# Optimization experiments

Hardware: AMD Instinct MI355X
Metric: run time of the kernel (lower is better)

Reference implementation:

```python
import jax, jax.numpy as jnp
import numpy as np

EPS = 1e-15


def setup_inputs() -> dict:
    key = jax.random.key(0)
    k1, k2 = jax.random.split(key)
    B, N, M, D = 32, 512, 64, 128  # D=128 hard-coded in original (np.zeros(128))
    videos_repr = jax.random.normal(k1, (B, N, D), dtype=jnp.float32)
    sentences_repr = jax.random.normal(k2, (B, M, D), dtype=jnp.float32)
    return {"videos_repr": videos_repr, "sentences_repr": sentences_repr}


def reference(videos_repr, sentences_repr):
    """Vectorized all-pairs (training=True) path of MomentVideo.call.

    videos_repr: [B, N, D], sentences_repr: [B, M, D].
    Returns (sum_scores_videos [B,B], sum_scores_sentences [B,B]).
    """
    V, S = videos_repr, sentences_repr
    nv = jnp.linalg.norm(V, axis=-1)  # [B, N]
    ns = jnp.linalg.norm(S, axis=-1)  # [B, M]

    # Co-attention cosine-similarity matrix for every (video i, sentence j) pair.
    # C[i,j,n,m] = <V[i,n], S[j,m]> / (||V[i,n]|| * ||S[j,m]|| + eps)
    C = jnp.einsum('ind,jmd->ijnm', V, S) / (
        nv[:, None, :, None] * ns[None, :, None, :] + EPS)

    Ps = jax.nn.softmax(C, axis=3)  # softmax over sentence words (axis=1 in per-pair matrix)
    Pv = jax.nn.softmax(C, axis=2)  # softmax over video segments (axis=0 in per-pair matrix)

    # sentence_attention[i,j,n] = sum_m Ps[i,j,n,m] * S[j,m]
    A = jnp.einsum('ijnm,jmd->ijnd', Ps, S)   # [B, B, N, D]
    # video_attention[i,j,m] = sum_n Pv[i,j,n,m] * V[i,n]
    Bt = jnp.einsum('ijnm,ind->ijmd', Pv, V)  # [B, B, M, D]

    na = jnp.linalg.norm(A, axis=-1)   # [B, B, N]
    nb = jnp.linalg.norm(Bt, axis=-1)  # [B, B, M]

    # cosine(V[i,n], A[i,j,n]) and cosine(S[j,m], Bt[i,j,m])
    sv = jnp.einsum('ind,ijnd->ijn', V, A) / (nv[:, None, :] * na + EPS)
    ss = jnp.einsum('jmd,ijmd->ijm', S, Bt) / (ns[None, :, :] * nb + EPS)

    sum_scores_videos = sv.mean(axis=-1)          # [B, B], [i, j]
    sum_scores_sentences = ss.mean(axis=-1).T     # transposed as in original
    return sum_scores_videos, sum_scores_sentences
```

## Files before the change

### kernel.cpp

```cpp
#include <hip/hip_runtime.h>
#include <hip/hip_bf16.h>
#include <math.h>

#define BB 32
#define NN 512
#define MM 64
#define DD 128
#define TILE 64
#define NTILES 8

typedef __attribute__((ext_vector_type(8))) short s8v;
typedef __attribute__((ext_vector_type(4))) float f4v;
typedef __attribute__((ext_vector_type(4))) unsigned short u4v;
typedef __attribute__((ext_vector_type(8))) unsigned short u8v;

#define MFMA(a, b, c) __builtin_amdgcn_mfma_f32_16x16x32_bf16((a), (b), (c), 0, 0, 0)

__device__ inline unsigned short f2b(float f) {
  union { __hip_bfloat16 b; unsigned short u; } cv;
  cv.b = __float2bfloat16(f);
  return cv.u;
}

__device__ inline int idxV(int r, int k)  { return r * 128 + (k ^ ((r & 7) << 3)); }
__device__ inline int idx64(int r, int k) { return r * 64  + (k ^ ((r & 7) << 3)); }

struct __align__(16) PSM {
  unsigned short A[64 * 128];
  unsigned short B[128 * 64];
};

extern "C" __global__ void __launch_bounds__(512, 2)
mv_prep(const float* __restrict__ Vg, const float* __restrict__ Sg,
        unsigned short* __restrict__ VAg, unsigned short* __restrict__ VTg,
        unsigned short* __restrict__ Sbg, unsigned short* __restrict__ Gbg,
        float* __restrict__ nvg, float* __restrict__ rnvg,
        float* __restrict__ nsg, float* __restrict__ rnsg)
{
  extern __shared__ char smraw[];
  PSM& sm = *reinterpret_cast<PSM*>(smraw);
  const int t = threadIdx.x;
  const int r = t >> 3, c = t & 7;
  const int bid = blockIdx.x;

  if (bid < 256) {
    const int i = bid >> 3, tt = bid & 7;
    const float* Vr = Vg + ((size_t)i * NN + tt * TILE + r) * DD + c * 16;
    float4 f0 = reinterpret_cast<const float4*>(Vr)[0];
    float4 f1 = reinterpret_cast<const float4*>(Vr)[1];
    float4 f2 = reinterpret_cast<const float4*>(Vr)[2];
    float4 f3 = reinterpret_cast<const float4*>(Vr)[3];
    unsigned short vb16[16] = {
      f2b(f0.x), f2b(f0.y), f2b(f0.z), f2b(f0.w),
      f2b(f1.x), f2b(f1.y), f2b(f1.z), f2b(f1.w),
      f2b(f2.x), f2b(f2.y), f2b(f2.z), f2b(f2.w),
      f2b(f3.x), f2b(f3.y), f2b(f3.z), f2b(f3.w) };
    u8v lo = { vb16[0], vb16[1], vb16[2], vb16[3], vb16[4], vb16[5], vb16[6], vb16[7] };
    u8v hi = { vb16[8], vb16[9], vb16[10], vb16[11], vb16[12], vb16[13], vb16[14], vb16[15] };
    *reinterpret_cast<u8v*>(&sm.A[idxV(r, c * 16)])     = lo;
    *reinterpret_cast<u8v*>(&sm.A[idxV(r, c * 16 + 8)]) = hi;
    #pragma unroll
    for (int q = 0; q < 8; ++q) {
      const int adr = ((c * 16 + q) << 6) + (r ^ (((q ^ c) & 7) << 3));
      sm.B[adr]       = vb16[q];
      sm.B[adr + 512] = vb16[q + 8];
    }
    float s = f0.x*f0.x + f0.y*f0.y + f0.z*f0.z + f0.w*f0.w
            + f1.x*f1.x + f1.y*f1.y + f1.z*f1.z + f1.w*f1.w
            + f2.x*f2.x + f2.y*f2.y + f2.z*f2.z + f2.w*f2.w
            + f3.x*f3.x + f3.y*f3.y + f3.z*f3.z + f3.w*f3.w;
    s += __shfl_xor(s, 1, 64);
    s += __shfl_xor(s, 2, 64);
    s += __shfl_xor(s, 4, 64);
    if (c == 0) {
      const float rs = rsqrtf(s);
      nvg [i * NN + tt * TILE + r] = s * rs;
      rnvg[i * NN + tt * TILE + r] = rs;
    }
    __syncthreads();
    unsigned short* dA = VAg + (size_t)bid * 8192;
    unsigned short* dB = VTg + (size_t)bid * 8192;
    *reinterpret_cast<u8v*>(&dA[t * 8])        = *reinterpret_cast<u8v*>(&sm.A[t * 8]);
    *reinterpret_cast<u8v*>(&dA[4096 + t * 8]) = *reinterpret_cast<u8v*>(&sm.A[4096 + t * 8]);
    *reinterpret_cast<u8v*>(&dB[t * 8])        = *reinterpret_cast<u8v*>(&sm.B[t * 8]);
    *reinterpret_cast<u8v*>(&dB[4096 + t * 8]) = *reinterpret_cast<u8v*>(&sm.B[4096 + t * 8]);
  } else {
    const int j = bid - 256;
    const float* Sp = Sg + ((size_t)j * MM + r) * DD + c * 16;
    float4 f0 = reinterpret_cast<const float4*>(Sp)[0];
    float4 f1 = reinterpret_cast<const float4*>(Sp)[1];
    float4 f2 = reinterpret_cast<const float4*>(Sp)[2];
    float4 f3 = reinterpret_cast<const float4*>(Sp)[3];
    u8v lo = { f2b(f0.x), f2b(f0.y), f2b(f0.z), f2b(f0.w),
               f2b(f1.x), f2b(f1.y), f2b(f1.z), f2b(f1.w) };
    u8v hi = { f2b(f2.x), f2b(f2.y), f2b(f2.z), f2b(f2.w),
               f2b(f3.x), f2b(f3.y), f2b(f3.z), f2b(f3.w) };
    *reinterpret_cast<u8v*>(&sm.A[idxV(r, c * 16)])     = lo;
    *reinterpret_cast<u8v*>(&sm.A[idxV(r, c * 16 + 8)]) = hi;
    float s = f0.x*f0.x + f0.y*f0.y + f0.z*f0.z + f0.w*f0.w
            + f1.x*f1.x + f1.y*f1.y + f1.z*f1.z + f1.w*f1.w
            + f2.x*f2.x + f2.y*f2.y + f2.z*f2.z + f2.w*f2.w
            + f3.x*f3.x + f3.y*f3.y + f3.z*f3.z + f3.w*f3.w;
    s += __shfl_xor(s, 1, 64);
    s += __shfl_xor(s, 2, 64);
    s += __shfl_xor(s, 4, 64);
    if (c == 0) {
      const float rs = rsqrtf(s);
      nsg [j * MM + r] = s * rs;
      rnsg[j * MM + r] = rs;
    }
    __syncthreads();
    {
      const int lane = t & 63, w = t >> 6, l15 = lane & 15, g = lane >> 4;
      const int nb = w >> 1, hf = w & 1, cB0 = hf * 32 + l15, cB1 = cB0 + 16;
      f4v g0 = {0.f,0.f,0.f,0.f}, g1 = {0.f,0.f,0.f,0.f};
      #pragma unroll
      for (int ks = 0; ks < 4; ++ks) {
        s8v a  = *reinterpret_cast<const s8v*>(&sm.A[idxV(nb * 16 + l15, ks * 32 + g * 8)]);
        s8v b0 = *reinterpret_cast<const s8v*>(&sm.A[idxV(cB0,          ks * 32 + g * 8)]);
        s8v b1 = *reinterpret_cast<const s8v*>(&sm.A[idxV(cB1,          ks * 32 + g * 8)]);
        g0 = MFMA(a, b0, g0);
        g1 = MFMA(a, b1, g1);
      }
      #pragma unroll
      for (int q = 0; q < 4; ++q) {
        const int row = nb * 16 + g * 4 + q;
        sm.B[idx64(row, cB0)] = f2b(g0[q]);
        sm.B[idx64(row, cB1)] = f2b(g1[q]);
      }
    }
    __syncthreads();
    unsigned short* dS = Sbg + (size_t)j * 8192;
    *reinterpret_cast<u8v*>(&dS[r * 128 + c * 16])     = *reinterpret_cast<u8v*>(&sm.A[idxV(r, c * 16)]);
    *reinterpret_cast<u8v*>(&dS[r * 128 + c * 16 + 8]) = *reinterpret_cast<u8v*>(&sm.A[idxV(r, c * 16 + 8)]);
    unsigned short* dG = Gbg + (size_t)j * 4096;
    *reinterpret_cast<u8v*>(&dG[r * 64 + c * 8]) = *reinterpret_cast<u8v*>(&sm.B[idx64(r, c * 8)]);
  }
}

struct __align__(16) SMem2 {
  unsigned short VA[8192];
  unsigned short VT[8192];
  unsigned short Eb[4096];
  unsigned short ET[4096];
  float RSV[32 * 68];
  float RQP[32 * 68];
  float RS [8 * 68];
  float nv_lds[512];
  float rnv_lds[512];
};

extern "C" __global__ void __launch_bounds__(512, 2)
mv_main(const unsigned short* __restrict__ VAg, const unsigned short* __restrict__ VTg,
        const unsigned short* __restrict__ Sbg, const unsigned short* __restrict__ Gbg,
        const float* __restrict__ nvg, const float* __restrict__ rnvg,
        const float* __restrict__ nsg, const float* __restrict__ rnsg,
        float* __restrict__ out)
{
  extern __shared__ char smraw[];
  SMem2& sm = *reinterpret_cast<SMem2*>(smraw);

  const int t    = threadIdx.x;
  const int lane = t & 63;
  const int w    = t >> 6;
  const int l15  = lane & 15;
  const int g    = lane >> 4;
  const int bi   = blockIdx.x >> 5;
  const int bj   = blockIdx.x & 31;

  const int nb  = w >> 1;
  const int hf  = w & 1;
  const int cB0 = hf * 32 + l15;
  const int cB1 = cB0 + 16;

  sm.nv_lds[t]  = nvg [bi * NN + t];
  sm.rnv_lds[t] = rnvg[bi * NN + t];

  s8v sfr0[4], sfr1[4], gfr0[2], gfr1[2];
  {
    const unsigned short* Sj = Sbg + (size_t)bj * 8192;
    #pragma unroll
    for (int ks = 0; ks < 4; ++ks) {
      sfr0[ks] = *reinterpret_cast<const s8v*>(&Sj[cB0 * 128 + ks * 32 + g * 8]);
      sfr1[ks] = *reinterpret_cast<const s8v*>(&Sj[cB1 * 128 + ks * 32 + g * 8]);
    }
    const unsigned short* Gj = Gbg + (size_t)bj * 4096;
    #pragma unroll
    for (int ks = 0; ks < 2; ++ks) {
      gfr0[ks] = *reinterpret_cast<const s8v*>(&Gj[cB0 * 64 + ks * 32 + g * 8]);
      gfr1[ks] = *reinterpret_cast<const s8v*>(&Gj[cB1 * 64 + ks * 32 + g * 8]);
    }
  }
  const float rns0r = rnsg[bj * MM + cB0];
  const float rns1r = rnsg[bj * MM + cB1];

  const unsigned short* VAi = VAg + (size_t)(bi * 8) * 8192;
  const unsigned short* VTi = VTg + (size_t)(bi * 8) * 8192;
  u8v p0 = *reinterpret_cast<const u8v*>(&VAi[t * 8]);
  u8v p1 = *reinterpret_cast<const u8v*>(&VAi[4096 + t * 8]);
  u8v p2 = *reinterpret_cast<const u8v*>(&VTi[t * 8]);
  u8v p3 = *reinterpret_cast<const u8v*>(&VTi[4096 + t * 8]);

  f4v bt4[4] = {{0.f,0.f,0.f,0.f},{0.f,0.f,0.f,0.f},{0.f,0.f,0.f,0.f},{0.f,0.f,0.f,0.f}};
  float svacc = 0.f, ssacc = 0.f;

  #pragma unroll 1
  for (int tt = 0; tt < NTILES; ++tt) {
    __syncthreads();
    *reinterpret_cast<u8v*>(&sm.VA[t * 8])        = p0;
    *reinterpret_cast<u8v*>(&sm.VA[4096 + t * 8]) = p1;
    *reinterpret_cast<u8v*>(&sm.VT[t * 8])        = p2;
    *reinterpret_cast<u8v*>(&sm.VT[4096 + t * 8]) = p3;
    if (tt < 7) {
      const unsigned short* a = VAi + (size_t)(tt + 1) * 8192;
      const unsigned short* b = VTi + (size_t)(tt + 1) * 8192;
      p0 = *reinterpret_cast<const u8v*>(&a[t * 8]);
      p1 = *reinterpret_cast<const u8v*>(&a[4096 + t * 8]);
      p2 = *reinterpret_cast<const u8v*>(&b[t * 8]);
      p3 = *reinterpret_cast<const u8v*>(&b[4096 + t * 8]);
    }
    if (tt > 0 && t < 64) {
      const int rg = t >> 2, qq = t & 3, hh = t >> 5;
      float sv_n = 0.f, qf = 0.f;
      #pragma unroll
      for (int l = 0; l < 16; ++l) {
        sv_n += sm.RSV[rg * 68 + l * 4 + qq] + sm.RSV[(16 + rg) * 68 + l * 4 + qq];
        qf   += sm.RQP[rg * 68 + l * 4 + qq] + sm.RQP[(16 + rg) * 68 + l * 4 + qq];
      }
      svacc += sv_n / (sm.nv_lds[(tt - 1) * TILE + t] * sqrtf(qf));
      float ssn = 0.f;
      #pragma unroll
      for (int n2 = 0; n2 < 4; ++n2) ssn += sm.RS[(n2 * 2 + hh) * 68 + t];
      ssacc += ssn;
    }
    __syncthreads();

    f4v a0 = {0.f,0.f,0.f,0.f}, a1 = {0.f,0.f,0.f,0.f};
    {
      const int ar = nb * 16 + l15;
      #pragma unroll
      for (int ks = 0; ks < 4; ++ks) {
        s8v av = *reinterpret_cast<const s8v*>(&sm.VA[idxV(ar, ks * 32 + g * 8)]);
        a0 = MFMA(av, sfr0[ks], a0);
        a1 = MFMA(av, sfr1[ks], a1);
      }
    }
    float e0[4], e1[4];
    {
      const float4 rv = *reinterpret_cast<const float4*>(&sm.rnv_lds[tt * TILE + nb * 16 + g * 4]);
      float sv4[4];
      float ss0 = 0.f, ss1 = 0.f;
      unsigned short eb0[4], eb1[4];
      #pragma unroll
      for (int q = 0; q < 4; ++q) {
        const float rvq = (q == 0) ? rv.x : (q == 1) ? rv.y : (q == 2) ? rv.z : rv.w;
        const float c0 = a0[q] * (rvq * rns0r);
        const float c1 = a1[q] * (rvq * rns1r);
        const float e0q = __expf(c0);
        const float e1q = __expf(c1);
        const float w0 = e0q * a0[q], w1 = e1q * a1[q];
        sv4[q] = w0 + w1;
        ss0 += w0; ss1 += w1;
        eb0[q] = f2b(e0q); eb1[q] = f2b(e1q);
        const int row = nb * 16 + g * 4 + q;
        sm.Eb[idx64(row, cB0)] = eb0[q];
        sm.Eb[idx64(row, cB1)] = eb1[q];
        e0[q] = e0q; e1[q] = e1q;
      }
      u4v et0 = { eb0[0], eb0[1], eb0[2], eb0[3] };
      u4v et1 = { eb1[0], eb1[1], eb1[2], eb1[3] };
      *reinterpret_cast<u4v*>(&sm.ET[idx64(cB0, nb * 16 + g * 4)]) = et0;
      *reinterpret_cast<u4v*>(&sm.ET[idx64(cB1, nb * 16 + g * 4)]) = et1;
      *reinterpret_cast<float4*>(&sm.RSV[(hf * 16 + nb * 4 + g) * 68 + l15 * 4]) =
          make_float4(sv4[0], sv4[1], sv4[2], sv4[3]);
      ss0 += __shfl_xor(ss0, 16, 64);  ss0 += __shfl_xor(ss0, 32, 64);
      ss1 += __shfl_xor(ss1, 16, 64);  ss1 += __shfl_xor(ss1, 32, 64);
      if (g == 0) { sm.RS[w * 68 + cB0] = ss0; sm.RS[w * 68 + cB1] = ss1; }
    }
    __syncthreads();

    {
      f4v fa0 = {0.f,0.f,0.f,0.f}, fa1 = {0.f,0.f,0.f,0.f};
      #pragma unroll
      for (int ks = 0; ks < 2; ++ks) {
        s8v ea = *reinterpret_cast<const s8v*>(&sm.Eb[idx64(nb * 16 + l15, ks * 32 + g * 8)]);
        fa0 = MFMA(ea, gfr0[ks], fa0);
        fa1 = MFMA(ea, gfr1[ks], fa1);
      }
      *reinterpret_cast<float4*>(&sm.RQP[(hf * 16 + nb * 4 + g) * 68 + l15 * 4]) =
          make_float4(e0[0]*fa0[0] + e1[0]*fa1[0], e0[1]*fa0[1] + e1[1]*fa1[1],
                      e0[2]*fa0[2] + e1[2]*fa1[2], e0[3]*fa0[3] + e1[3]*fa1[3]);
    }
    {
      const int xr = l15 & 7;
      #pragma unroll
      for (int ks = 0; ks < 2; ++ks) {
        s8v pa = *reinterpret_cast<const s8v*>(&sm.ET[idx64(nb * 16 + l15, ks * 32 + g * 8)]);
        const int k0 = ks * 32 + g * 8;
        #pragma unroll
        for (int dt = 0; dt < 4; ++dt) {
          const int rowv = (hf * 4 + dt) * 16 + l15;
          const int elem = (rowv << 6) + (k0 ^ (((xr ^ (hf * 4 + dt)) & 7) << 3));
          s8v vb = *reinterpret_cast<const s8v*>(&sm.VT[elem]);
          bt4[dt] = MFMA(pa, vb, bt4[dt]);
        }
      }
    }
  }

  __syncthreads();
  if (t < 64) {
    const int rg = t >> 2, qq = t & 3, hh = t >> 5;
    float sv_n = 0.f, qf = 0.f;
    #pragma unroll
    for (int l = 0; l < 16; ++l) {
      sv_n += sm.RSV[rg * 68 + l * 4 + qq] + sm.RSV[(16 + rg) * 68 + l * 4 + qq];
      qf   += sm.RQP[rg * 68 + l * 4 + qq] + sm.RQP[(16 + rg) * 68 + l * 4 + qq];
    }
    svacc += sv_n / (sm.nv_lds[7 * TILE + t] * sqrtf(qf));
    float ssn = 0.f;
    #pragma unroll
    for (int n2 = 0; n2 < 4; ++n2) ssn += sm.RS[(n2 * 2 + hh) * 68 + t];
    ssacc += ssn;
  }
  __syncthreads();
  {
    float bq[4];
    #pragma unroll
    for (int q = 0; q < 4; ++q)
      bq[q] = bt4[0][q]*bt4[0][q] + bt4[1][q]*bt4[1][q]
            + bt4[2][q]*bt4[2][q] + bt4[3][q]*bt4[3][q];
    *reinterpret_cast<float4*>(&sm.RQP[(hf * 16 + nb * 4 + g) * 68 + l15 * 4]) =
        make_float4(bq[0], bq[1], bq[2], bq[3]);
  }
  __syncthreads();
  if (t < 64) {
    const int rg = t >> 2, qq = t & 3;
    float btq = 0.f;
    #pragma unroll
    for (int l = 0; l < 16; ++l)
      btq += sm.RQP[rg * 68 + l * 4 + qq] + sm.RQP[(16 + rg) * 68 + l * 4 + qq];
    float ssv = ssacc / (nsg[bj * MM + t] * sqrtf(btq));
    float svv = svacc;
    #pragma unroll
    for (int msk = 32; msk >= 1; msk >>= 1) {
      ssv += __shfl_xor(ssv, msk, 64);
      svv += __shfl_xor(svv, msk, 64);
    }
    if (t == 0) {
      out[bi * BB + bj]           = svv * (1.0f / NN);
      out[BB * BB + bj * BB + bi] = ssv * (1.0f / MM);
    }
  }
}

extern "C" void kernel_launch(void* const* d_in, const int* in_sizes, int n_in,
                              void* d_out, int out_size, void* d_ws, size_t ws_size,
                              hipStream_t stream) {
  const float* V = (const float*)d_in[0];
  const float* S = (const float*)d_in[1];
  float* out = (float*)d_out;

  char* ws = (char*)d_ws;
  unsigned short* VAg = (unsigned short*)(ws + 0);
  unsigned short* VTg = (unsigned short*)(ws + 4194304);
  unsigned short* Sbg = (unsigned short*)(ws + 8388608);
  unsigned short* Gbg = (unsigned short*)(ws + 8912896);
  float* nvg  = (float*)(ws + 9175040);
  float* rnvg = (float*)(ws + 9240576);
  float* nsg  = (float*)(ws + 9306112);
  float* rnsg = (float*)(ws + 9314304);

  static_assert(sizeof(PSM)  <= 160 * 1024, "prep LDS");
  static_assert(sizeof(SMem2) <= 80 * 1024, "main LDS: need 2 blocks/CU");
  hipFuncSetAttribute(reinterpret_cast<const void*>(mv_prep),
                      hipFuncAttributeMaxDynamicSharedMemorySize, (int)sizeof(PSM));
  hipFuncSetAttribute(reinterpret_cast<const void*>(mv_main),
                      hipFuncAttributeMaxDynamicSharedMemorySize, (int)sizeof(SMem2));

  mv_prep<<<dim3(288), dim3(512), sizeof(PSM), stream>>>(
      V, S, VAg, VTg, Sbg, Gbg, nvg, rnvg, nsg, rnsg);
  mv_main<<<dim3(BB * BB), dim3(512), sizeof(SMem2), stream>>>(
      VAg, VTg, Sbg, Gbg, nvg, rnvg, nsg, rnsg, out);
}
```

Baseline: 132.4 us.

## Shrink LDS via wave-shuffle row reductions to fit three blocks per CU

Replaces the 32x68 float LDS staging buffers for per-row sv and qp partial sums with in-wave xor-shuffle reductions, so only 2x64 floats are written to LDS. This removes the 64-thread serial 16-step LDS reduction loops and the nv_lds buffer, and swaps divisions by sqrt for multiplies with precomputed reciprocals and rsqrtf. LDS footprint drops enough to request three 512-thread blocks per CU via launch bounds, which also tightens the register budget and may cause spills. The extra shuffles add work across all waves in exchange for less serial tail work and higher occupancy.

```diff
diff --git a/kernel.cpp b/kernel.cpp
--- a/kernel.cpp
+++ b/kernel.cpp
@@ -143,14 +143,13 @@
   unsigned short VT[8192];
   unsigned short Eb[4096];
   unsigned short ET[4096];
-  float RSV[32 * 68];
-  float RQP[32 * 68];
+  float RSV[2][64];
+  float RQP[2][64];
   float RS [8 * 68];
-  float nv_lds[512];
   float rnv_lds[512];
 };
 
-extern "C" __global__ void __launch_bounds__(512, 2)
+extern "C" __global__ void __launch_bounds__(512, 3)
 mv_main(const unsigned short* __restrict__ VAg, const unsigned short* __restrict__ VTg,
         const unsigned short* __restrict__ Sbg, const unsigned short* __restrict__ Gbg,
         const float* __restrict__ nvg, const float* __restrict__ rnvg,
@@ -173,7 +172,6 @@
   const int cB0 = hf * 32 + l15;
   const int cB1 = cB0 + 16;
 
-  sm.nv_lds[t]  = nvg [bi * NN + t];
   sm.rnv_lds[t] = rnvg[bi * NN + t];
 
   s8v sfr0[4], sfr1[4], gfr0[2], gfr1[2];
@@ -220,14 +218,10 @@
       p3 = *reinterpret_cast<const u8v*>(&b[4096 + t * 8]);
     }
     if (tt > 0 && t < 64) {
-      const int rg = t >> 2, qq = t & 3, hh = t >> 5;
-      float sv_n = 0.f, qf = 0.f;
-      #pragma unroll
-      for (int l = 0; l < 16; ++l) {
-        sv_n += sm.RSV[rg * 68 + l * 4 + qq] + sm.RSV[(16 + rg) * 68 + l * 4 + qq];
-        qf   += sm.RQP[rg * 68 + l * 4 + qq] + sm.RQP[(16 + rg) * 68 + l * 4 + qq];
-      }
-      svacc += sv_n / (sm.nv_lds[(tt - 1) * TILE + t] * sqrtf(qf));
+      const float sv_n = sm.RSV[0][t] + sm.RSV[1][t];
+      const float qf   = sm.RQP[0][t] + sm.RQP[1][t];
+      svacc += sv_n * sm.rnv_lds[(tt - 1) * TILE + t] * rsqrtf(qf);
+      const int hh = t >> 5;
       float ssn = 0.f;
       #pragma unroll
       for (int n2 = 0; n2 < 4; ++n2) ssn += sm.RS[(n2 * 2 + hh) * 68 + t];
@@ -271,8 +265,15 @@
       u4v et1 = { eb1[0], eb1[1], eb1[2], eb1[3] };
       *reinterpret_cast<u4v*>(&sm.ET[idx64(cB0, nb * 16 + g * 4)]) = et0;
       *reinterpret_cast<u4v*>(&sm.ET[idx64(cB1, nb * 16 + g * 4)]) = et1;
-      *reinterpret_cast<float4*>(&sm.RSV[(hf * 16 + nb * 4 + g) * 68 + l15 * 4]) =
-          make_float4(sv4[0], sv4[1], sv4[2], sv4[3]);
+      #pragma unroll
+      for (int msk = 1; msk <= 8; msk <<= 1) {
+        #pragma unroll
+        for (int q = 0; q < 4; ++q) sv4[q] += __shfl_xor(sv4[q], msk, 64);
+      }
+      if (l15 == 0) {
+        #pragma unroll
+        for (int q = 0; q < 4; ++q) sm.RSV[hf][nb * 16 + g * 4 + q] = sv4[q];
+      }
       ss0 += __shfl_xor(ss0, 16, 64);  ss0 += __shfl_xor(ss0, 32, 64);
       ss1 += __shfl_xor(ss1, 16, 64);  ss1 += __shfl_xor(ss1, 32, 64);
       if (g == 0) { sm.RS[w * 68 + cB0] = ss0; sm.RS[w * 68 + cB1] = ss1; }
@@ -287,9 +288,18 @@
         fa0 = MFMA(ea, gfr0[ks], fa0);
         fa1 = MFMA(ea, gfr1[ks], fa1);
       }
-      *reinterpret_cast<float4*>(&sm.RQP[(hf * 16 + nb * 4 + g) * 68 + l15 * 4]) =
-          make_float4(e0[0]*fa0[0] + e1[0]*fa1[0], e0[1]*fa0[1] + e1[1]*fa1[1],
-                      e0[2]*fa0[2] + e1[2]*fa1[2], e0[3]*fa0[3] + e1[3]*fa1[3]);
+      float qp[4];
+      #pragma unroll
+      for (int q = 0; q < 4; ++q) qp[q] = e0[q]*fa0[q] + e1[q]*fa1[q];
+      #pragma unroll
+      for (int msk = 1; msk <= 8; msk <<= 1) {
+        #pragma unroll
+        for (int q = 0; q < 4; ++q) qp[q] += __shfl_xor(qp[q], msk, 64);
+      }
+      if (l15 == 0) {
+        #pragma unroll
+        for (int q = 0; q < 4; ++q) sm.RQP[hf][nb * 16 + g * 4 + q] = qp[q];
+      }
     }
     {
       const int xr = l15 & 7;
@@ -310,14 +320,10 @@
 
   __syncthreads();
   if (t < 64) {
-    const int rg = t >> 2, qq = t & 3, hh = t >> 5;
-    float sv_n = 0.f, qf = 0.f;
-    #pragma unroll
-    for (int l = 0; l < 16; ++l) {
-      sv_n += sm.RSV[rg * 68 + l * 4 + qq] + sm.RSV[(16 + rg) * 68 + l * 4 + qq];
-      qf   += sm.RQP[rg * 68 + l * 4 + qq] + sm.RQP[(16 + rg) * 68 + l * 4 + qq];
-    }
-    svacc += sv_n / (sm.nv_lds[7 * TILE + t] * sqrtf(qf));
+    const float sv_n = sm.RSV[0][t] + sm.RSV[1][t];
+    const float qf   = sm.RQP[0][t] + sm.RQP[1][t];
+    svacc += sv_n * sm.rnv_lds[7 * TILE + t] * rsqrtf(qf);
+    const int hh = t >> 5;
     float ssn = 0.f;
     #pragma unroll
     for (int n2 = 0; n2 < 4; ++n2) ssn += sm.RS[(n2 * 2 + hh) * 68 + t];
@@ -330,17 +336,20 @@
     for (int q = 0; q < 4; ++q)
       bq[q] = bt4[0][q]*bt4[0][q] + bt4[1][q]*bt4[1][q]
             + bt4[2][q]*bt4[2][q] + bt4[3][q]*bt4[3][q];
-    *reinterpret_cast<float4*>(&sm.RQP[(hf * 16 + nb * 4 + g) * 68 + l15 * 4]) =
-        make_float4(bq[0], bq[1], bq[2], bq[3]);
+    #pragma unroll
+    for (int msk = 1; msk <= 8; msk <<= 1) {
+      #pragma unroll
+      for (int q = 0; q < 4; ++q) bq[q] += __shfl_xor(bq[q], msk, 64);
+    }
+    if (l15 == 0) {
+      #pragma unroll
+      for (int q = 0; q < 4; ++q) sm.RQP[hf][nb * 16 + g * 4 + q] = bq[q];
+    }
   }
   __syncthreads();
   if (t < 64) {
-    const int rg = t >> 2, qq = t & 3;
-    float btq = 0.f;
-    #pragma unroll
-    for (int l = 0; l < 16; ++l)
-      btq += sm.RQP[rg * 68 + l * 4 + qq] + sm.RQP[(16 + rg) * 68 + l * 4 + qq];
-    float ssv = ssacc / (nsg[bj * MM + t] * sqrtf(btq));
+    const float btq = sm.RQP[0][t] + sm.RQP[1][t];
+    float ssv = ssacc * rnsg[bj * MM + t] * rsqrtf(btq);
     float svv = svacc;
     #pragma unroll
     for (int msk = 32; msk >= 1; msk >>= 1) {
@@ -372,7 +381,7 @@
   float* rnsg = (float*)(ws + 9314304);
 
   static_assert(sizeof(PSM)  <= 160 * 1024, "prep LDS");
-  static_assert(sizeof(SMem2) <= 80 * 1024, "main LDS: need 2 blocks/CU");
+  static_assert(sizeof(SMem2) <= 54613, "main LDS: need 3 blocks/CU");
   hipFuncSetAttribute(reinterpret_cast<const void*>(mv_prep),
                       hipFuncAttributeMaxDynamicSharedMemorySize, (int)sizeof(PSM));
   hipFuncSetAttribute(reinterpret_cast<const void*>(mv_main),
```

Result: slower. 139.2 us (+5.2%).
